# Kernel tuning notes

Measured on AMD Instinct MI355X. Metric: run time of the kernel, lower is better.

Reference implementation:

```python
import jax, jax.numpy as jnp
import numpy as np

B, N, D = 8, 2048, 1024


def setup_inputs() -> dict:
    key = jax.random.key(0)
    k1, k2, k3, k4 = jax.random.split(key, 4)
    x = jax.random.normal(k1, (B, N, D), dtype=jnp.float32)
    f = jax.random.normal(k2, (B, N, D), dtype=jnp.float32)
    # nn.Linear(D, 1, bias=False) weights, shape [1, D]
    lim = 1.0 / np.sqrt(D)
    wk = jax.random.uniform(k3, (1, D), dtype=jnp.float32, minval=-lim, maxval=lim)
    wq = jax.random.uniform(k4, (1, D), dtype=jnp.float32, minval=-lim, maxval=lim)
    return {"x": x, "f": f, "wk": wk, "wq": wq}


def reference(x, f, wk, wq):
    # scalar k/q projections: [B, N]
    k = jnp.einsum("bnd,d->bn", x, wk[0])
    q = jnp.einsum("bnd,d->bn", x, wq[0])
    scale = 1.0 / jnp.sqrt(jnp.float32(D))
    # rank-1 outer-product scores: e[b,i,j] = k[b,i]*q[b,j]/sqrt(D)
    e = k[:, :, None] * q[:, None, :] * scale  # [B, N, N]
    # keep upper triangle (incl. diag), then any exact zero -> -inf
    # (faithful to torch: e_post[e_post == 0] = -inf, which also hits
    #  naturally-zero upper-triangle entries)
    e_tri = jnp.triu(e)
    e_post = jnp.where(e_tri == 0, -jnp.inf, e_tri)
    a = jax.nn.softmax(e_post, axis=1)  # softmax over rows (dim=1)
    # f_out = a^T @ f
    f_out = jnp.einsum("bij,bid->bjd", a, f)
    return f_out
```

## Files before the change

kernel.cpp:

```cpp
#include <hip/hip_runtime.h>

#define B 8
#define N 2048
#define D 1024
#define C 16
#define LC (N / C)
#define M 6
#define NBLK (B * C * 2)
#define RECF (M * 512)


__global__ __launch_bounds__(256) void k_proj(const float* __restrict__ x,
                                              const float* __restrict__ wk,
                                              const float* __restrict__ wq,
                                              float* __restrict__ kq,
                                              int* __restrict__ flags) {
    if (blockIdx.x == 0) flags[threadIdx.x] = 0;

    const int wave = threadIdx.x >> 6;
    const int lane = threadIdx.x & 63;
    const int row  = blockIdx.x * 4 + wave;
    const float4* xr  = (const float4*)(x + (size_t)row * D);
    const float4* wk4 = (const float4*)wk;
    const float4* wq4 = (const float4*)wq;
    float ak = 0.f, aq = 0.f;
#pragma unroll
    for (int t = 0; t < (D / 4) / 64; ++t) {
        float4 xv = xr[t * 64 + lane];
        float4 kv = wk4[t * 64 + lane];
        float4 qv = wq4[t * 64 + lane];
        ak += xv.x * kv.x + xv.y * kv.y + xv.z * kv.z + xv.w * kv.w;
        aq += xv.x * qv.x + xv.y * qv.y + xv.z * qv.z + xv.w * qv.w;
    }
#pragma unroll
    for (int off = 32; off > 0; off >>= 1) {
        ak += __shfl_down(ak, off, 64);
        aq += __shfl_down(aq, off, 64);
    }
    if (lane == 0) {
        kq[row] = ak;
        kq[B * N + row] = aq;
    }
}

__global__ __launch_bounds__(256, 4) void k_fused(
    const float* __restrict__ kq, const float* __restrict__ f,
    float* __restrict__ precs, int* __restrict__ flags,
    float* __restrict__ out)
{
    const int bid   = blockIdx.x;
    const int dh    = bid & 1;
    const int c     = (bid >> 1) & (C - 1);
    const int b     = bid >> 5;
    const int chain = b * 2 + dh;
    const int tid   = threadIdx.x;
    const int d     = dh * 512 + tid * 2;

    __shared__ float sk[LC];
    __shared__ float sq[LC];
    __shared__ float sT[M];

    if (tid < 128) sk[tid]       = kq[b * N + c * LC + tid];
    else           sq[tid - 128] = kq[B * N + b * N + c * LC + (tid - 128)];
    __syncthreads();

    const float2* fb = (const float2*)(f + (size_t)(b * N + c * LC) * D + d);
    float2 s[M];
#pragma unroll
    for (int m = 0; m < M; ++m) s[m] = make_float2(0.f, 0.f);
#pragma unroll 8
    for (int i = 0; i < LC; ++i) {
        float2 ff = fb[i * (D / 2)];
        float  kk = sk[i];
        float  w  = (kk != 0.0f) ? 1.0f : 0.0f;
        s[0].x += w * ff.x; s[0].y += w * ff.y;
        float kp = kk;
#pragma unroll
        for (int m = 1; m < M; ++m) {
            s[m].x += kp * ff.x; s[m].y += kp * ff.y;
            kp *= kk;
        }
    }

    if (c < C - 1) {
        float* rec = precs + (size_t)(chain * C + c) * RECF;
#pragma unroll
        for (int m = 0; m < M; ++m)
            ((float2*)(rec + m * 512))[tid] = s[m];
        __syncthreads();
        if (tid == 0) {
            __threadfence();
            __hip_atomic_store(&flags[chain * C + c], 1,
                               __ATOMIC_RELAXED, __HIP_MEMORY_SCOPE_AGENT);
        }
    }

    if (tid < C) {
        float tm[M] = {0.f, 0.f, 0.f, 0.f, 0.f, 0.f};
        const float* kb = kq + b * N + tid * LC;
#pragma unroll 8
        for (int i = 0; i < LC; ++i) {
            float kk = kb[i];
            tm[0] += (kk != 0.0f) ? 1.0f : 0.0f;
            float kp = kk;
#pragma unroll
            for (int m = 1; m < M; ++m) { tm[m] += kp; kp *= kk; }
        }
#pragma unroll
        for (int m = 0; m < M; ++m) {
            float v = tm[m];
            const float orig = v;
#pragma unroll
            for (int off = 1; off < C; off <<= 1) {
                float nv = __shfl_up(v, off, 64);
                if (tid >= off) v += nv;
            }
            if (tid == c) sT[m] = v - orig;
        }
    }

    float2 run[M];
#pragma unroll
    for (int m = 0; m < M; ++m) run[m] = make_float2(0.f, 0.f);

    if (c > 0) {
        if (tid < c) {
            while (__hip_atomic_load(&flags[chain * C + tid],
                                     __ATOMIC_RELAXED, __HIP_MEMORY_SCOPE_AGENT) == 0)
                __builtin_amdgcn_s_sleep(2);
        }
        __syncthreads();
        (void)__hip_atomic_load(&flags[chain * C],
                                __ATOMIC_ACQUIRE, __HIP_MEMORY_SCOPE_AGENT);
        for (int p = 0; p < c; ++p) {
            const float* rp = precs + (size_t)(chain * C + p) * RECF;
#pragma unroll
            for (int m = 0; m < M; ++m) {
                float2 v = ((const float2*)(rp + m * 512))[tid];
                run[m].x += v.x; run[m].y += v.y;
            }
        }
    }
    __syncthreads();

    float t[M];
#pragma unroll
    for (int m = 0; m < M; ++m) t[m] = sT[m];

    float2* ob = (float2*)(out + (size_t)(b * N + c * LC) * D + d);
#pragma unroll 4
    for (int i = 0; i < LC; ++i) {
        float2 ff = fb[i * (D / 2)];
        float  kk = sk[i];
        float  qq = sq[i];
        float  w  = (kk != 0.0f) ? 1.0f : 0.0f;
        t[0] += w;
        run[0].x += w * ff.x; run[0].y += w * ff.y;
        float kp = kk;
#pragma unroll
        for (int m = 1; m < M; ++m) {
            t[m] += kp;
            run[m].x += kp * ff.x; run[m].y += kp * ff.y;
            kp *= kk;
        }
        const float cj = qq * 0.03125f;
        const float g2 = cj * 0.5f;
        const float g3 = cj * (1.0f / 3.0f);
        const float g4 = cj * 0.25f;
        const float g5 = cj * 0.2f;
        float Z = ((((t[5] * g5 + t[4]) * g4 + t[3]) * g3 + t[2]) * g2 + t[1]) * cj + t[0];
        float rz = __builtin_amdgcn_rcpf(Z);
        float2 o;
        o.x = (((((run[5].x * g5 + run[4].x) * g4 + run[3].x) * g3 + run[2].x) * g2 + run[1].x) * cj + run[0].x) * rz;
        o.y = (((((run[5].y * g5 + run[4].y) * g4 + run[3].y) * g3 + run[2].y) * g2 + run[1].y) * cj + run[0].y) * rz;
        ob[i * (D / 2)] = o;
    }
}

extern "C" void kernel_launch(void* const* d_in, const int* in_sizes, int n_in,
                              void* d_out, int out_size, void* d_ws, size_t ws_size,
                              hipStream_t stream) {
    (void)in_sizes; (void)n_in; (void)out_size; (void)ws_size;
    const float* x  = (const float*)d_in[0];
    const float* f  = (const float*)d_in[1];
    const float* wk = (const float*)d_in[2];
    const float* wq = (const float*)d_in[3];
    float* out = (float*)d_out;
    float* ws  = (float*)d_ws;

    float* kq    = ws;
    int*   flags = (int*)(ws + 32768);
    float* precs = ws + 33792;

    hipLaunchKernelGGL(k_proj,  dim3(B * N / 4), dim3(256), 0, stream, x, wk, wq, kq, flags);
    hipLaunchKernelGGL(k_fused, dim3(NBLK),      dim3(256), 0, stream, kq, f, precs, flags, out);
}
```

Baseline: 210.4 us.

## Fuse projection into single persistent kernel with epoch flags and finer chunking

Merges the k/q projection kernel into the main scan kernel. Each block computes 16 rows of k/q, then spins on per-batch epoch flags before building its chunk prefix sums. Chunk count doubles to 32, and the D split goes from halves to quarters with one float per thread instead of float2. This removes a kernel launch and increases block count for parallelism. The cost is extra cross-block spin-waits, narrower per-thread loads, and reliance on all 1024 blocks being co-resident.

```diff
diff --git a/kernel.cpp b/kernel.cpp
--- a/kernel.cpp
+++ b/kernel.cpp
@@ -3,97 +3,130 @@
 #define B 8
 #define N 2048
 #define D 1024
-#define C 16
+#define C 32
 #define LC (N / C)
 #define M 6
-#define NBLK (B * C * 2)
-#define RECF (M * 512)
-
-
-__global__ __launch_bounds__(256) void k_proj(const float* __restrict__ x,
-                                              const float* __restrict__ wk,
-                                              const float* __restrict__ wq,
-                                              float* __restrict__ kq,
-                                              int* __restrict__ flags) {
-    if (blockIdx.x == 0) flags[threadIdx.x] = 0;
-
-    const int wave = threadIdx.x >> 6;
-    const int lane = threadIdx.x & 63;
-    const int row  = blockIdx.x * 4 + wave;
-    const float4* xr  = (const float4*)(x + (size_t)row * D);
-    const float4* wk4 = (const float4*)wk;
-    const float4* wq4 = (const float4*)wq;
-    float ak = 0.f, aq = 0.f;
-#pragma unroll
-    for (int t = 0; t < (D / 4) / 64; ++t) {
-        float4 xv = xr[t * 64 + lane];
-        float4 kv = wk4[t * 64 + lane];
-        float4 qv = wq4[t * 64 + lane];
-        ak += xv.x * kv.x + xv.y * kv.y + xv.z * kv.z + xv.w * kv.w;
-        aq += xv.x * qv.x + xv.y * qv.y + xv.z * qv.z + xv.w * qv.w;
-    }
-#pragma unroll
-    for (int off = 32; off > 0; off >>= 1) {
-        ak += __shfl_down(ak, off, 64);
-        aq += __shfl_down(aq, off, 64);
-    }
-    if (lane == 0) {
-        kq[row] = ak;
-        kq[B * N + row] = aq;
-    }
-}
-
-__global__ __launch_bounds__(256, 4) void k_fused(
-    const float* __restrict__ kq, const float* __restrict__ f,
-    float* __restrict__ precs, int* __restrict__ flags,
+#define DQ 4
+#define COLS (D / DQ)
+#define NBLK (B * C * DQ)
+#define TPB 256
+#define RECF (M * COLS)
+
+__device__ unsigned g_ctr;
+__device__ int g_flagP[B * C * DQ];
+__device__ int g_flagA[B * DQ * C];
+
+
+__global__ __launch_bounds__(TPB, 4) void k_all(
+    const float* __restrict__ x, const float* __restrict__ f,
+    const float* __restrict__ wk, const float* __restrict__ wq,
+    float* __restrict__ kq, float* __restrict__ precs,
     float* __restrict__ out)
 {
     const int bid   = blockIdx.x;
-    const int dh    = bid & 1;
-    const int c     = (bid >> 1) & (C - 1);
-    const int b     = bid >> 5;
-    const int chain = b * 2 + dh;
+    const int dq    = bid & (DQ - 1);
+    const int c     = (bid >> 2) & (C - 1);
+    const int b     = bid >> 7;
+    const int chain = b * DQ + dq;
     const int tid   = threadIdx.x;
-    const int d     = dh * 512 + tid * 2;
+    const int wave  = tid >> 6;
+    const int lane  = tid & 63;
 
     __shared__ float sk[LC];
     __shared__ float sq[LC];
     __shared__ float sT[M];
-
-    if (tid < 128) sk[tid]       = kq[b * N + c * LC + tid];
-    else           sq[tid - 128] = kq[B * N + b * N + c * LC + (tid - 128)];
-    __syncthreads();
-
-    const float2* fb = (const float2*)(f + (size_t)(b * N + c * LC) * D + d);
-    float2 s[M];
-#pragma unroll
-    for (int m = 0; m < M; ++m) s[m] = make_float2(0.f, 0.f);
+    __shared__ int   s_ep;
+
+    if (tid == 0) s_ep = (int)(atomicAdd(&g_ctr, 1u) / NBLK) + 1;
+    __syncthreads();
+    const int ep = s_ep;
+
+    {
+        const float4* wk4 = (const float4*)wk;
+        const float4* wq4 = (const float4*)wq;
+        float4 kw[4], qw[4];
+#pragma unroll
+        for (int t = 0; t < 4; ++t) { kw[t] = wk4[t * 64 + lane]; qw[t] = wq4[t * 64 + lane]; }
+#pragma unroll
+        for (int r = 0; r < 4; ++r) {
+            const int row = c * LC + dq * 16 + wave * 4 + r;
+            const float4* xr = (const float4*)(x + ((size_t)(b * N + row)) * D);
+            float ak = 0.f, aq = 0.f;
+#pragma unroll
+            for (int t = 0; t < 4; ++t) {
+                float4 xv = xr[t * 64 + lane];
+                ak += xv.x * kw[t].x + xv.y * kw[t].y + xv.z * kw[t].z + xv.w * kw[t].w;
+                aq += xv.x * qw[t].x + xv.y * qw[t].y + xv.z * qw[t].z + xv.w * qw[t].w;
+            }
+#pragma unroll
+            for (int off = 32; off > 0; off >>= 1) {
+                ak += __shfl_down(ak, off, 64);
+                aq += __shfl_down(aq, off, 64);
+            }
+            if (lane == 0) {
+                kq[b * N + row] = ak;
+                kq[B * N + b * N + row] = aq;
+            }
+        }
+    }
+    __syncthreads();
+    if (tid == 0) {
+        __threadfence();
+        __hip_atomic_store(&g_flagP[(b * C + c) * DQ + dq], ep,
+                           __ATOMIC_RELAXED, __HIP_MEMORY_SCOPE_AGENT);
+    }
+
+    if (tid < DQ) {
+        while (__hip_atomic_load(&g_flagP[(b * C + c) * DQ + tid],
+                                 __ATOMIC_RELAXED, __HIP_MEMORY_SCOPE_AGENT) != ep)
+            __builtin_amdgcn_s_sleep(2);
+    }
+    __syncthreads();
+    (void)__hip_atomic_load(&g_flagP[(b * C + c) * DQ],
+                            __ATOMIC_ACQUIRE, __HIP_MEMORY_SCOPE_AGENT);
+    if (tid < LC)            sk[tid]      = kq[b * N + c * LC + tid];
+    else if (tid < 2 * LC)   sq[tid - LC] = kq[B * N + b * N + c * LC + (tid - LC)];
+    __syncthreads();
+
+    const int d = dq * COLS + tid;
+    const float* fb = f + ((size_t)(b * N + c * LC)) * D + d;
+    float s[M] = {0.f, 0.f, 0.f, 0.f, 0.f, 0.f};
 #pragma unroll 8
     for (int i = 0; i < LC; ++i) {
-        float2 ff = fb[i * (D / 2)];
-        float  kk = sk[i];
-        float  w  = (kk != 0.0f) ? 1.0f : 0.0f;
-        s[0].x += w * ff.x; s[0].y += w * ff.y;
+        float ff = fb[(size_t)i * D];
+        float kk = sk[i];
+        float w  = (kk != 0.0f) ? 1.0f : 0.0f;
+        s[0] += w * ff;
         float kp = kk;
 #pragma unroll
-        for (int m = 1; m < M; ++m) {
-            s[m].x += kp * ff.x; s[m].y += kp * ff.y;
-            kp *= kk;
-        }
+        for (int m = 1; m < M; ++m) { s[m] += kp * ff; kp *= kk; }
     }
 
     if (c < C - 1) {
         float* rec = precs + (size_t)(chain * C + c) * RECF;
 #pragma unroll
-        for (int m = 0; m < M; ++m)
-            ((float2*)(rec + m * 512))[tid] = s[m];
+        for (int m = 0; m < M; ++m) rec[m * COLS + tid] = s[m];
         __syncthreads();
         if (tid == 0) {
             __threadfence();
-            __hip_atomic_store(&flags[chain * C + c], 1,
+            __hip_atomic_store(&g_flagA[chain * C + c], ep,
                                __ATOMIC_RELAXED, __HIP_MEMORY_SCOPE_AGENT);
         }
     }
+
+    if (tid < C * DQ) {
+        while (__hip_atomic_load(&g_flagP[b * C * DQ + tid],
+                                 __ATOMIC_RELAXED, __HIP_MEMORY_SCOPE_AGENT) != ep)
+            __builtin_amdgcn_s_sleep(2);
+    }
+    if (tid < c) {
+        while (__hip_atomic_load(&g_flagA[chain * C + tid],
+                                 __ATOMIC_RELAXED, __HIP_MEMORY_SCOPE_AGENT) != ep)
+            __builtin_amdgcn_s_sleep(2);
+    }
+    __syncthreads();
+    (void)__hip_atomic_load(&g_flagP[b * C * DQ],
+                            __ATOMIC_ACQUIRE, __HIP_MEMORY_SCOPE_AGENT);
 
     if (tid < C) {
         float tm[M] = {0.f, 0.f, 0.f, 0.f, 0.f, 0.f};
@@ -119,27 +152,12 @@
         }
     }
 
-    float2 run[M];
-#pragma unroll
-    for (int m = 0; m < M; ++m) run[m] = make_float2(0.f, 0.f);
-
-    if (c > 0) {
-        if (tid < c) {
-            while (__hip_atomic_load(&flags[chain * C + tid],
-                                     __ATOMIC_RELAXED, __HIP_MEMORY_SCOPE_AGENT) == 0)
-                __builtin_amdgcn_s_sleep(2);
-        }
-        __syncthreads();
-        (void)__hip_atomic_load(&flags[chain * C],
-                                __ATOMIC_ACQUIRE, __HIP_MEMORY_SCOPE_AGENT);
-        for (int p = 0; p < c; ++p) {
-            const float* rp = precs + (size_t)(chain * C + p) * RECF;
-#pragma unroll
-            for (int m = 0; m < M; ++m) {
-                float2 v = ((const float2*)(rp + m * 512))[tid];
-                run[m].x += v.x; run[m].y += v.y;
-            }
-        }
+    float run[M] = {0.f, 0.f, 0.f, 0.f, 0.f, 0.f};
+#pragma unroll 1
+    for (int p = 0; p < c; ++p) {
+        const float* rp = precs + (size_t)(chain * C + p) * RECF;
+#pragma unroll
+        for (int m = 0; m < M; ++m) run[m] += rp[m * COLS + tid];
     }
     __syncthreads();
 
@@ -147,20 +165,20 @@
 #pragma unroll
     for (int m = 0; m < M; ++m) t[m] = sT[m];
 
-    float2* ob = (float2*)(out + (size_t)(b * N + c * LC) * D + d);
+    float* ob = out + ((size_t)(b * N + c * LC)) * D + d;
 #pragma unroll 4
     for (int i = 0; i < LC; ++i) {
-        float2 ff = fb[i * (D / 2)];
-        float  kk = sk[i];
-        float  qq = sq[i];
-        float  w  = (kk != 0.0f) ? 1.0f : 0.0f;
+        float ff = fb[(size_t)i * D];
+        float kk = sk[i];
+        float qq = sq[i];
+        float w  = (kk != 0.0f) ? 1.0f : 0.0f;
         t[0] += w;
-        run[0].x += w * ff.x; run[0].y += w * ff.y;
+        run[0] += w * ff;
         float kp = kk;
 #pragma unroll
         for (int m = 1; m < M; ++m) {
             t[m] += kp;
-            run[m].x += kp * ff.x; run[m].y += kp * ff.y;
+            run[m] += kp * ff;
             kp *= kk;
         }
         const float cj = qq * 0.03125f;
@@ -170,10 +188,8 @@
         const float g5 = cj * 0.2f;
         float Z = ((((t[5] * g5 + t[4]) * g4 + t[3]) * g3 + t[2]) * g2 + t[1]) * cj + t[0];
         float rz = __builtin_amdgcn_rcpf(Z);
-        float2 o;
-        o.x = (((((run[5].x * g5 + run[4].x) * g4 + run[3].x) * g3 + run[2].x) * g2 + run[1].x) * cj + run[0].x) * rz;
-        o.y = (((((run[5].y * g5 + run[4].y) * g4 + run[3].y) * g3 + run[2].y) * g2 + run[1].y) * cj + run[0].y) * rz;
-        ob[i * (D / 2)] = o;
+        ob[(size_t)i * D] =
+            (((((run[5] * g5 + run[4]) * g4 + run[3]) * g3 + run[2]) * g2 + run[1]) * cj + run[0]) * rz;
     }
 }
 
@@ -189,9 +205,8 @@
     float* ws  = (float*)d_ws;
 
     float* kq    = ws;
-    int*   flags = (int*)(ws + 32768);
-    float* precs = ws + 33792;
-
-    hipLaunchKernelGGL(k_proj,  dim3(B * N / 4), dim3(256), 0, stream, x, wk, wq, kq, flags);
-    hipLaunchKernelGGL(k_fused, dim3(NBLK),      dim3(256), 0, stream, kq, f, precs, flags, out);
+    float* precs = ws + 32768;
+
+    hipLaunchKernelGGL(k_all, dim3(NBLK), dim3(TPB), 0, stream,
+                       x, f, wk, wq, kq, precs, out);
 }
```

Measured after the change: 351.6 us. 67.1% more time.
